# Performance work log

Hardware: AMD Instinct MI355X
Metric: run time of the kernel (lower is better)

## Reference

```python
import jax, jax.numpy as jnp
import numpy as np

N_GRID = 5
ORDER = 3
X_MIN = -1.0
X_MAX = 1.0
N_BASIS = N_GRID + ORDER - 1  # 7
EPS = 1e-8


def _make_grid():
    # order repeated endpoints on each side of n_grid interior knots
    interior = jnp.linspace(X_MIN, X_MAX, N_GRID, dtype=jnp.float32)
    left = jnp.full((ORDER,), X_MIN, dtype=jnp.float32)
    right = jnp.full((ORDER,), X_MAX, dtype=jnp.float32)
    return jnp.concatenate([left, interior, right])  # (n_grid + 2*order,) = (11,)


def _b_spline_basis(xc, grid):
    """Vectorized Cox-de Boor over all input dims at once.
    xc: (N, d_in) clamped to [X_MIN, X_MAX]. Returns (N, d_in, N_BASIS)."""
    xe = xc[..., None]  # (N, d_in, 1)
    # degree-0 indicator basis on each knot interval
    basis = ((xe >= grid[:-1]) & (xe < grid[1:])).astype(xc.dtype)
    # right-closed last interval: x == grid[-1] counts for last basis
    basis = basis.at[..., -1].add((xc == grid[-1]).astype(xc.dtype))
    for k in range(1, ORDER + 1):
        n_k = grid.shape[0] - k - 1
        denom_l = jnp.maximum(grid[k:n_k + k] - grid[:n_k], EPS)
        coeff_l = (xe - grid[:n_k]) / denom_l
        denom_r = jnp.maximum(grid[k + 1:n_k + k + 1] - grid[1:n_k + 1], EPS)
        coeff_r = (grid[k + 1:n_k + k + 1] - xe) / denom_r
        basis = coeff_l * basis[..., :n_k] + coeff_r * basis[..., 1:n_k + 1]
    return basis  # (N, d_in, N_BASIS)


def setup_inputs() -> dict:
    key = jax.random.key(0)
    k1, k2, k3 = jax.random.split(key, 3)
    N, d_in, d_out = 8192, 1024, 1024
    x = jax.random.normal(k1, (N, d_in), dtype=jnp.float32)
    # coeff is zero-init in torch; use small random values so spline path is exercised
    coeff = jax.random.normal(k2, (d_out, d_in, N_BASIS), dtype=jnp.float32) * 0.1
    w_base = jax.random.normal(k3, (d_out, d_in), dtype=jnp.float32) * (1.0 / np.sqrt(d_in))
    bias = jnp.zeros((d_out,), dtype=jnp.float32)
    return {"x": x, "coeff": coeff, "w_base": w_base, "bias": bias}


def reference(x, coeff, w_base, bias):
    grid = _make_grid()
    xc = jnp.clip(x, X_MIN, X_MAX)               # (N, d_in)
    basis = _b_spline_basis(xc, grid)            # (N, d_in, n_basis)
    y_spline = jnp.einsum('nib,oib->no', basis, coeff)  # (N, d_out)
    y_base = jax.nn.silu(xc) @ w_base.T          # (N, d_out)
    return y_spline + y_base + bias
```

## Files before the change

### kernel.cpp

```cpp
#include <hip/hip_runtime.h>

#define D_IN   1024
#define D_OUT  1024
#define N_SLOT 8
#define KB_CNT (D_IN / 8)
#define IMG_BYTES 16384
#define COL_TILES (D_OUT / 128)

typedef __attribute__((ext_vector_type(8))) short bf16x8;
typedef __attribute__((ext_vector_type(4))) float f32x4;
typedef __attribute__((ext_vector_type(4))) unsigned int u32x4;

typedef __attribute__((address_space(1))) unsigned int as1_u32;
typedef __attribute__((address_space(3))) unsigned int as3_u32;

__device__ __forceinline__ void gload_lds16(const void* g, void* l) {
  __builtin_amdgcn_global_load_lds((const as1_u32*)(unsigned long long)g,
                                   (as3_u32*)(unsigned int)(unsigned long long)l,
                                   16, 0, 0);
}

__device__ __forceinline__ unsigned short f2bf(float f) {
  unsigned int u = __float_as_uint(f);
  u += 0x7fffu + ((u >> 16) & 1u);
  return (unsigned short)(u >> 16);
}

__device__ __forceinline__ float basis_and_silu(float xv, float* b) {
  float xc = fminf(fmaxf(xv, -1.f), 1.f);
  const float G[11] = {-1.f, -1.f, -1.f, -1.f, -0.5f, 0.f, 0.5f, 1.f, 1.f, 1.f, 1.f};
  float t[10];
#pragma unroll
  for (int j = 0; j < 10; j++)
    t[j] = (xc >= G[j] && xc < G[j + 1]) ? 1.f : 0.f;
  t[9] += (xc == 1.f) ? 1.f : 0.f;
#pragma unroll
  for (int k = 1; k <= 3; k++) {
#pragma unroll
    for (int j = 0; j < 10 - k; j++) {
      float dl = G[j + k] - G[j];
      float il = 1.f / (dl < 1e-8f ? 1e-8f : dl);
      float dr = G[j + k + 1] - G[j + 1];
      float ir = 1.f / (dr < 1e-8f ? 1e-8f : dr);
      t[j] = (xc - G[j]) * il * t[j] + (G[j + k + 1] - xc) * ir * t[j + 1];
    }
  }
#pragma unroll
  for (int j = 0; j < 7; j++) b[j] = t[j];
  return xc / (1.f + __expf(-xc));
}

__global__ __launch_bounds__(256) void prep_kernel(const float* __restrict__ coeff,
                                                   const float* __restrict__ w_base,
                                                   char* __restrict__ bp) {
  int tid = blockIdx.x * 256 + threadIdx.x;
  int o = tid >> 10;
  int i = tid & (D_IN - 1);

  float v[8];
#pragma unroll
  for (int b = 0; b < 7; b++) v[b] = coeff[(size_t)tid * 7 + b];
  v[7] = w_base[tid];

  union { unsigned short h[8]; u32x4 q; } u;
#pragma unroll
  for (int b = 0; b < 8; b++) u.h[b] = f2bf(v[b]);

  int tileC = o >> 7, cl = o & 127, kb = i >> 3, il = i & 7;
  size_t img = ((size_t)(tileC * KB_CNT + kb)) * IMG_BYTES;
  int off = (cl * 128 + il * 16) ^ ((cl & 7) << 4);
  *(u32x4*)(bp + img + off) = u.q;
}

__global__ __launch_bounds__(256) void act_kernel(const float* __restrict__ x,
                                                  char* __restrict__ ap) {
  int tid = blockIdx.x * 256 + threadIdx.x;
  int row = tid >> 10;
  int i = tid & (D_IN - 1);

  float b[7];
  float s = basis_and_silu(x[tid], b);

  union { unsigned short h[8]; u32x4 q; } u;
#pragma unroll
  for (int q2 = 0; q2 < 7; q2++) u.h[q2] = f2bf(b[q2]);
  u.h[7] = f2bf(s);

  int tile = row >> 7, r = row & 127, kb = i >> 3, il_ = i & 7;
  size_t img = ((size_t)(tile * KB_CNT + kb)) * IMG_BYTES;
  int off = (r * 128 + il_ * 16) ^ ((r & 7) << 4);
  *(u32x4*)(ap + img + off) = u.q;
}

__global__ __launch_bounds__(256, 2) void gemm_kernel(const char* __restrict__ ap,
                                                      const char* __restrict__ bp,
                                                      const float* __restrict__ bias,
                                                      float* __restrict__ out) {
  __shared__ __align__(16) char lds[32768];

  const int bid = blockIdx.x;
  const int tileR = bid >> 3;
  const int tileC = bid & (COL_TILES - 1);
  const int tid = threadIdx.x;
  const int lane = tid & 63;
  const int w = tid >> 6;
  const int wr = w >> 1, wc = w & 1;

  const char* ag = ap + (size_t)tileR * KB_CNT * IMG_BYTES + w * 4096 + lane * 16;
  const char* bg = bp + (size_t)tileC * KB_CNT * IMG_BYTES + w * 4096 + lane * 16;
  char* lA = lds + w * 4096;
  char* lB = lds + 16384 + w * 4096;

  f32x4 acc[4][4];
#pragma unroll
  for (int m = 0; m < 4; m++)
#pragma unroll
    for (int n = 0; n < 4; n++) acc[m][n] = (f32x4){0.f, 0.f, 0.f, 0.f};

  const int abase = (wr * 64 + (lane & 15)) * 128 + ((lane >> 4) * 16);
  const int bbase = (wc * 64 + (lane & 15)) * 128 + ((lane >> 4) * 16) + 16384;
  const int xorm = (lane & 7) << 4;

  for (int kb = 0; kb < KB_CNT; kb++) {
#pragma unroll
    for (int t = 0; t < 4; t++) gload_lds16(ag + t * 1024, lA + t * 1024);
#pragma unroll
    for (int t = 0; t < 4; t++) gload_lds16(bg + t * 1024, lB + t * 1024);
    ag += IMG_BYTES; bg += IMG_BYTES;
    __syncthreads();

#pragma unroll
    for (int kk = 0; kk < 2; kk++) {
      bf16x8 af[4], bfr[4];
#pragma unroll
      for (int m = 0; m < 4; m++)
        af[m] = *(const bf16x8*)(lds + ((abase + m * 2048 + kk * 64) ^ xorm));
#pragma unroll
      for (int n = 0; n < 4; n++)
        bfr[n] = *(const bf16x8*)(lds + ((bbase + n * 2048 + kk * 64) ^ xorm));
#pragma unroll
      for (int m = 0; m < 4; m++)
#pragma unroll
        for (int n = 0; n < 4; n++)
          acc[m][n] = __builtin_amdgcn_mfma_f32_16x16x32_bf16(af[m], bfr[n], acc[m][n], 0, 0, 0);
    }
    __syncthreads();
  }

  const int r0 = tileR * 128 + wr * 64 + ((lane >> 4) * 4);
  const int c0 = tileC * 128 + wc * 64 + (lane & 15);
#pragma unroll
  for (int m = 0; m < 4; m++) {
#pragma unroll
    for (int n = 0; n < 4; n++) {
      int c = c0 + n * 16;
      float bv = bias[c];
#pragma unroll
      for (int j = 0; j < 4; j++) {
        int r = r0 + m * 16 + j;
        out[(size_t)r * D_OUT + c] = acc[m][n][j] + bv;
      }
    }
  }
}

__global__ __launch_bounds__(256) void naive_kernel(const float* __restrict__ x,
                                                    const float* __restrict__ coeff,
                                                    const float* __restrict__ w_base,
                                                    const float* __restrict__ bias,
                                                    float* __restrict__ out) {
  __shared__ float sb[D_IN][8];
  const int n = blockIdx.x >> 2;
  const int o = (blockIdx.x & 3) * 256 + threadIdx.x;

  for (int i = threadIdx.x; i < D_IN; i += 256) {
    float b[7];
    float s = basis_and_silu(x[(size_t)n * D_IN + i], b);
#pragma unroll
    for (int q = 0; q < 7; q++) sb[i][q] = b[q];
    sb[i][7] = s;
  }
  __syncthreads();

  float acc = bias[o];
  for (int i = 0; i < D_IN; i++) {
    const float* cp = coeff + ((size_t)o * D_IN + i) * 7;
    float p = sb[i][7] * w_base[(size_t)o * D_IN + i];
#pragma unroll
    for (int q = 0; q < 7; q++) p += sb[i][q] * cp[q];
    acc += p;
  }
  out[(size_t)n * D_OUT + o] = acc;
}

extern "C" void kernel_launch(void* const* d_in, const int* in_sizes, int n_in,
                              void* d_out, int out_size, void* d_ws, size_t ws_size,
                              hipStream_t stream) {
  const float* x      = (const float*)d_in[0];
  const float* coeff  = (const float*)d_in[1];
  const float* w_base = (const float*)d_in[2];
  const float* bias   = (const float*)d_in[3];
  float* out = (float*)d_out;

  const int n_rows = in_sizes[0] / D_IN;
  const int row_tiles = n_rows / 128;

  const size_t bp_bytes = (size_t)COL_TILES * KB_CNT * IMG_BYTES;
  const size_t tile_bytes = (size_t)KB_CNT * IMG_BYTES;

  if (ws_size < bp_bytes + tile_bytes) {
    naive_kernel<<<n_rows * 4, 256, 0, stream>>>(x, coeff, w_base, bias, out);
    return;
  }

  char* bp = (char*)d_ws;
  char* apb = bp + bp_bytes;
  size_t avail = ws_size - bp_bytes;
  int chunk_tiles = (int)(avail / tile_bytes);
  if (chunk_tiles > row_tiles) chunk_tiles = row_tiles;

  prep_kernel<<<(D_OUT * D_IN) / 256, 256, 0, stream>>>(coeff, w_base, bp);

  for (int t0 = 0; t0 < row_tiles; t0 += chunk_tiles) {
    int nt = (row_tiles - t0 < chunk_tiles) ? (row_tiles - t0) : chunk_tiles;
    act_kernel<<<(nt * 128 * D_IN) / 256, 256, 0, stream>>>(
        x + (size_t)t0 * 128 * D_IN, apb);
    gemm_kernel<<<nt * COL_TILES, 256, 0, stream>>>(
        apb, bp, bias, out + (size_t)t0 * 128 * D_OUT);
  }
}
```

Before: 289.4 us.

## Rewrite GEMM as 8-wave 256x128 tile with triple-buffered LDS pipeline

Replaces the 256-thread 128x128 GEMM with a 512-thread kernel computing 256x128 output tiles. It uses a three-stage LDS ring buffer filled by direct global-to-LDS loads that are issued between MFMA phases, together with explicit waitcnt, barriers and setprio. Workgroup IDs are remapped so that neighbouring tiles land on the same XCD, which should improve L2 reuse. The activation kernel now has each thread load a float4 and handle four inputs. The goal is to hide global-load latency and raise MFMA utilisation, at the cost of much more LDS (144KB) and tricky synchronisation that must be correct.

New measurement: 277.6 us. 4.1% less time.

```diff
diff --git a/kernel.cpp b/kernel.cpp
--- a/kernel.cpp
+++ b/kernel.cpp
@@ -2,7 +2,6 @@
 
 #define D_IN   1024
 #define D_OUT  1024
-#define N_SLOT 8
 #define KB_CNT (D_IN / 8)
 #define IMG_BYTES 16384
 #define COL_TILES (D_OUT / 128)
@@ -75,41 +74,57 @@
 __global__ __launch_bounds__(256) void act_kernel(const float* __restrict__ x,
                                                   char* __restrict__ ap) {
   int tid = blockIdx.x * 256 + threadIdx.x;
-  int row = tid >> 10;
-  int i = tid & (D_IN - 1);
-
-  float b[7];
-  float s = basis_and_silu(x[tid], b);
-
-  union { unsigned short h[8]; u32x4 q; } u;
-#pragma unroll
-  for (int q2 = 0; q2 < 7; q2++) u.h[q2] = f2bf(b[q2]);
-  u.h[7] = f2bf(s);
-
-  int tile = row >> 7, r = row & 127, kb = i >> 3, il_ = i & 7;
-  size_t img = ((size_t)(tile * KB_CNT + kb)) * IMG_BYTES;
-  int off = (r * 128 + il_ * 16) ^ ((r & 7) << 4);
-  *(u32x4*)(ap + img + off) = u.q;
-}
-
-__global__ __launch_bounds__(256, 2) void gemm_kernel(const char* __restrict__ ap,
-                                                      const char* __restrict__ bp,
-                                                      const float* __restrict__ bias,
-                                                      float* __restrict__ out) {
-  __shared__ __align__(16) char lds[32768];
-
-  const int bid = blockIdx.x;
-  const int tileR = bid >> 3;
-  const int tileC = bid & (COL_TILES - 1);
+  int row = tid >> 8;
+  int iq = (tid & 255) * 4;
+
+  float4 xv = *(const float4*)(x + ((size_t)row << 10) + iq);
+  float xs[4] = {xv.x, xv.y, xv.z, xv.w};
+
+  int tile = row >> 7, r = row & 127;
+  int roff = r * 128;
+  int xorm = (r & 7) << 4;
+
+#pragma unroll
+  for (int e = 0; e < 4; e++) {
+    float b[7];
+    float s = basis_and_silu(xs[e], b);
+    union { unsigned short h[8]; u32x4 q; } u;
+#pragma unroll
+    for (int q2 = 0; q2 < 7; q2++) u.h[q2] = f2bf(b[q2]);
+    u.h[7] = f2bf(s);
+    int i = iq + e;
+    int kb = i >> 3, il = i & 7;
+    size_t img = ((size_t)(tile * KB_CNT + kb)) * IMG_BYTES;
+    int off = (roff + il * 16) ^ xorm;
+    *(u32x4*)(ap + img + off) = u.q;
+  }
+}
+
+#define BUFB 49152
+
+__global__ __launch_bounds__(512, 2) void gemm8_kernel(const char* __restrict__ ap,
+                                                       const char* __restrict__ bp,
+                                                       const float* __restrict__ bias,
+                                                       float* __restrict__ out) {
+  __shared__ __align__(16) char lds[3 * BUFB];
+
+  const int nwg = gridDim.x;
+  const int orig = blockIdx.x;
+  const int q = nwg >> 3, r = nwg & 7;
+  const int xcd = orig & 7, seq = orig >> 3;
+  const int wg = (xcd < r ? xcd * (q + 1) : r * (q + 1) + (xcd - r) * q) + seq;
+  const int tileR = wg >> 3;
+  const int tileC = wg & 7;
+
   const int tid = threadIdx.x;
   const int lane = tid & 63;
   const int w = tid >> 6;
-  const int wr = w >> 1, wc = w & 1;
-
-  const char* ag = ap + (size_t)tileR * KB_CNT * IMG_BYTES + w * 4096 + lane * 16;
-  const char* bg = bp + (size_t)tileC * KB_CNT * IMG_BYTES + w * 4096 + lane * 16;
-  char* lA = lds + w * 4096;
-  char* lB = lds + 16384 + w * 4096;
+  const int wm = w >> 1, wn = w & 1;
+
+  const char* pa0 = ap + ((size_t)(tileR * 2 + 0) * KB_CNT) * IMG_BYTES + tid * 16;
+  const char* pa1 = ap + ((size_t)(tileR * 2 + 1) * KB_CNT) * IMG_BYTES + tid * 16;
+  const char* pb  = bp + ((size_t)tileC * KB_CNT) * IMG_BYTES + tid * 16;
+  char* lw = lds + w * 1024;
 
   f32x4 acc[4][4];
 #pragma unroll
@@ -117,38 +132,91 @@
 #pragma unroll
     for (int n = 0; n < 4; n++) acc[m][n] = (f32x4){0.f, 0.f, 0.f, 0.f};
 
-  const int abase = (wr * 64 + (lane & 15)) * 128 + ((lane >> 4) * 16);
-  const int bbase = (wc * 64 + (lane & 15)) * 128 + ((lane >> 4) * 16) + 16384;
-  const int xorm = (lane & 7) << 4;
-
-  for (int kb = 0; kb < KB_CNT; kb++) {
-#pragma unroll
-    for (int t = 0; t < 4; t++) gload_lds16(ag + t * 1024, lA + t * 1024);
-#pragma unroll
-    for (int t = 0; t < 4; t++) gload_lds16(bg + t * 1024, lB + t * 1024);
-    ag += IMG_BYTES; bg += IMG_BYTES;
-    __syncthreads();
-
-#pragma unroll
-    for (int kk = 0; kk < 2; kk++) {
-      bf16x8 af[4], bfr[4];
-#pragma unroll
-      for (int m = 0; m < 4; m++)
-        af[m] = *(const bf16x8*)(lds + ((abase + m * 2048 + kk * 64) ^ xorm));
-#pragma unroll
-      for (int n = 0; n < 4; n++)
-        bfr[n] = *(const bf16x8*)(lds + ((bbase + n * 2048 + kk * 64) ^ xorm));
-#pragma unroll
-      for (int m = 0; m < 4; m++)
-#pragma unroll
-        for (int n = 0; n < 4; n++)
-          acc[m][n] = __builtin_amdgcn_mfma_f32_16x16x32_bf16(af[m], bfr[n], acc[m][n], 0, 0, 0);
-    }
-    __syncthreads();
-  }
-
-  const int r0 = tileR * 128 + wr * 64 + ((lane >> 4) * 4);
-  const int c0 = tileC * 128 + wc * 64 + (lane & 15);
+  const int xm = (lane & 7) << 4;
+  const int arow = wm * 64 + (lane & 15);
+  const int bcol = wn * 64 + (lane & 15);
+  const int kch = (lane >> 4) * 16;
+
+#pragma unroll
+  for (int ss = 0; ss < 2; ++ss) {
+    gload_lds16(pa0,        lw + ss * BUFB);
+    gload_lds16(pa0 + 8192, lw + ss * BUFB + 8192);
+    gload_lds16(pa1,        lw + ss * BUFB + 16384);
+    gload_lds16(pa1 + 8192, lw + ss * BUFB + 24576);
+    gload_lds16(pb,         lw + ss * BUFB + 32768);
+    gload_lds16(pb + 8192,  lw + ss * BUFB + 40960);
+    pa0 += IMG_BYTES; pa1 += IMG_BYTES; pb += IMG_BYTES;
+  }
+  asm volatile("s_waitcnt vmcnt(6)" ::: "memory");
+  __builtin_amdgcn_s_barrier();
+
+  int bsel = 0, ssel = 2;
+  for (int t = 0; t < KB_CNT; ++t) {
+    const char* lb = lds + bsel * BUFB;
+    char* sw = lw + ssel * BUFB;
+    const bool stg = (t + 2) < KB_CNT;
+    bf16x8 af[2][2], bfr[4][2], ag[2][2];
+
+#pragma unroll
+    for (int c = 0; c < 2; ++c) {
+      af[c][0] = *(const bf16x8*)(lb + (((arow + c * 16) * 128 + kch) ^ xm));
+      af[c][1] = *(const bf16x8*)(lb + (((arow + c * 16) * 128 + 64 + kch) ^ xm));
+    }
+#pragma unroll
+    for (int n = 0; n < 4; ++n) {
+      bfr[n][0] = *(const bf16x8*)(lb + 32768 + (((bcol + n * 16) * 128 + kch) ^ xm));
+      bfr[n][1] = *(const bf16x8*)(lb + 32768 + (((bcol + n * 16) * 128 + 64 + kch) ^ xm));
+    }
+    if (stg) {
+      gload_lds16(pa0,        sw);
+      gload_lds16(pa0 + 8192, sw + 8192);
+      gload_lds16(pa1,        sw + 16384);
+    }
+    __builtin_amdgcn_s_barrier();
+    asm volatile("s_waitcnt lgkmcnt(0)" ::: "memory");
+    __builtin_amdgcn_s_setprio(1);
+#pragma unroll
+    for (int c = 0; c < 2; ++c)
+#pragma unroll
+      for (int n = 0; n < 4; ++n) {
+        acc[c][n] = __builtin_amdgcn_mfma_f32_16x16x32_bf16(af[c][0], bfr[n][0], acc[c][n], 0, 0, 0);
+        acc[c][n] = __builtin_amdgcn_mfma_f32_16x16x32_bf16(af[c][1], bfr[n][1], acc[c][n], 0, 0, 0);
+      }
+    __builtin_amdgcn_s_setprio(0);
+    __builtin_amdgcn_s_barrier();
+
+#pragma unroll
+    for (int c = 0; c < 2; ++c) {
+      ag[c][0] = *(const bf16x8*)(lb + (((arow + (c + 2) * 16) * 128 + kch) ^ xm));
+      ag[c][1] = *(const bf16x8*)(lb + (((arow + (c + 2) * 16) * 128 + 64 + kch) ^ xm));
+    }
+    if (stg) {
+      gload_lds16(pa1 + 8192, sw + 24576);
+      gload_lds16(pb,         sw + 32768);
+      gload_lds16(pb + 8192,  sw + 40960);
+    }
+    if (t < KB_CNT - 2) { asm volatile("s_waitcnt vmcnt(6)" ::: "memory"); }
+    else                { asm volatile("s_waitcnt vmcnt(0)" ::: "memory"); }
+    __builtin_amdgcn_s_barrier();
+    asm volatile("s_waitcnt lgkmcnt(0)" ::: "memory");
+    __builtin_amdgcn_s_setprio(1);
+#pragma unroll
+    for (int c = 0; c < 2; ++c)
+#pragma unroll
+      for (int n = 0; n < 4; ++n) {
+        acc[c + 2][n] = __builtin_amdgcn_mfma_f32_16x16x32_bf16(ag[c][0], bfr[n][0], acc[c + 2][n], 0, 0, 0);
+        acc[c + 2][n] = __builtin_amdgcn_mfma_f32_16x16x32_bf16(ag[c][1], bfr[n][1], acc[c + 2][n], 0, 0, 0);
+      }
+    __builtin_amdgcn_s_setprio(0);
+    __builtin_amdgcn_s_barrier();
+
+    if (stg) { pa0 += IMG_BYTES; pa1 += IMG_BYTES; pb += IMG_BYTES; }
+    bsel = bsel == 2 ? 0 : bsel + 1;
+    ssel = ssel == 2 ? 0 : ssel + 1;
+  }
+
+  const int r0 = tileR * 256 + wm * 64 + ((lane >> 4) * 4);
+  const int c0 = tileC * 128 + wn * 64 + (lane & 15);
 #pragma unroll
   for (int m = 0; m < 4; m++) {
 #pragma unroll
@@ -157,8 +225,8 @@
       float bv = bias[c];
 #pragma unroll
       for (int j = 0; j < 4; j++) {
-        int r = r0 + m * 16 + j;
-        out[(size_t)r * D_OUT + c] = acc[m][n][j] + bv;
+        int rr = r0 + m * 16 + j;
+        out[(size_t)rr * D_OUT + c] = acc[m][n][j] + bv;
       }
     }
   }
@@ -177,7 +245,7 @@
     float b[7];
     float s = basis_and_silu(x[(size_t)n * D_IN + i], b);
 #pragma unroll
-    for (int q = 0; q < 7; q++) sb[i][q] = b[q];
+    for (int qd = 0; qd < 7; qd++) sb[i][qd] = b[qd];
     sb[i][7] = s;
   }
   __syncthreads();
@@ -187,7 +255,7 @@
     const float* cp = coeff + ((size_t)o * D_IN + i) * 7;
     float p = sb[i][7] * w_base[(size_t)o * D_IN + i];
 #pragma unroll
-    for (int q = 0; q < 7; q++) p += sb[i][q] * cp[q];
+    for (int qd = 0; qd < 7; qd++) p += sb[i][qd] * cp[qd];
     acc += p;
   }
   out[(size_t)n * D_OUT + o] = acc;
@@ -208,24 +276,23 @@
   const size_t bp_bytes = (size_t)COL_TILES * KB_CNT * IMG_BYTES;
   const size_t tile_bytes = (size_t)KB_CNT * IMG_BYTES;
 
-  if (ws_size < bp_bytes + tile_bytes) {
+  if (ws_size < bp_bytes + 2 * tile_bytes) {
     naive_kernel<<<n_rows * 4, 256, 0, stream>>>(x, coeff, w_base, bias, out);
     return;
   }
 
-  char* bp = (char*)d_ws;
-  char* apb = bp + bp_bytes;
+  char* bpw = (char*)d_ws;
+  char* apb = bpw + bp_bytes;
   size_t avail = ws_size - bp_bytes;
-  int chunk_tiles = (int)(avail / tile_bytes);
+  int chunk_tiles = (int)(avail / tile_bytes) & ~1;
   if (chunk_tiles > row_tiles) chunk_tiles = row_tiles;
 
-  prep_kernel<<<(D_OUT * D_IN) / 256, 256, 0, stream>>>(coeff, w_base, bp);
+  prep_kernel<<<(D_OUT * D_IN) / 256, 256, 0, stream>>>(coeff, w_base, bpw);
 
   for (int t0 = 0; t0 < row_tiles; t0 += chunk_tiles) {
     int nt = (row_tiles - t0 < chunk_tiles) ? (row_tiles - t0) : chunk_tiles;
-    act_kernel<<<(nt * 128 * D_IN) / 256, 256, 0, stream>>>(
-        x + (size_t)t0 * 128 * D_IN, apb);
-    gemm_kernel<<<nt * COL_TILES, 256, 0, stream>>>(
-        apb, bp, bias, out + (size_t)t0 * 128 * D_OUT);
-  }
-}
+    act_kernel<<<nt * 128, 256, 0, stream>>>(x + (size_t)t0 * 128 * D_IN, apb);
+    gemm8_kernel<<<(nt / 2) * COL_TILES, 512, 0, stream>>>(
+        apb, bpw, bias, out + (size_t)t0 * 128 * D_OUT);
+  }
+}
```
